# Kernel optimization log

Measured on AMD Instinct MI355X. Metric: run time of the kernel, lower is better.

## Reference

```python
import jax, jax.numpy as jnp
import numpy as np

SIGMA = 1.0  # kernel bandwidth (init kwarg)

VS = 4096   # src vertices
VT = 4096   # tar vertices
FS = 8192   # src triangles
FT = 8192   # tar triangles
FR = 8192   # reference triangles


def setup_inputs() -> dict:
    key = jax.random.key(0)
    k0, k1, k2, k3, k4, k5 = jax.random.split(key, 6)
    src_vertices = jax.random.normal(k0, (VS, 3), dtype=jnp.float32)
    src_indices = jax.random.randint(k1, (FS, 3), 0, VS, dtype=jnp.int64)
    tar_vertices = jax.random.normal(k2, (VT, 3), dtype=jnp.float32)
    tar_indices = jax.random.randint(k3, (FT, 3), 0, VT, dtype=jnp.int64)
    ref_normals = 0.1 * jax.random.normal(k4, (FR, 3), dtype=jnp.float32)
    ref_centers = jax.random.normal(k5, (FR, 3), dtype=jnp.float32)
    return {
        "src_vertices": src_vertices,
        "src_indices": src_indices,
        "tar_vertices": tar_vertices,
        "tar_indices": tar_indices,
        "ref_normals": ref_normals,
        "ref_centers": ref_centers,
    }


def _tri_normals_centers(vertices, indices):
    tris = vertices[indices]               # [F, 3, 3]
    a, b, c = tris[:, 0, :], tris[:, 1, :], tris[:, 2, :]
    normals = 0.5 * jnp.cross(a - b, c - b)  # [F, 3]
    centers = tris.sum(axis=1) / 3.0         # [F, 3]
    return normals, centers


def _sqdist(src, tar):
    # d[i, j] = ||tar_i - src_j||^2  -> shape [Nt, Ns]
    s2 = jnp.sum(src * src, axis=-1)  # [Ns]
    t2 = jnp.sum(tar * tar, axis=-1)  # [Nt]
    return t2[:, None] + s2[None, :] - 2.0 * (tar @ src.T)


def _cauchy(d):
    return 1.0 / (1.0 + d / SIGMA) ** 2


def _energy(sn, sc, tn, tc):
    e1 = jnp.sum((sn @ sn.T) * _cauchy(_sqdist(sc, sc)))
    e2 = jnp.sum((tn @ sn.T) * _cauchy(_sqdist(sc, tc)))
    e3 = jnp.sum((tn @ tn.T) * _cauchy(_sqdist(tc, tc)))
    return e1 - 2.0 * e2 + e3


def reference(src_vertices, src_indices, tar_vertices, tar_indices, ref_normals, ref_centers):
    src_n, src_c = _tri_normals_centers(src_vertices, src_indices)
    tar_n, tar_c = _tri_normals_centers(tar_vertices, tar_indices)
    energy = _energy(src_n, src_c, ref_normals, ref_centers)
    energy = energy + _energy(tar_n, tar_c, ref_normals, ref_centers)
    energy = energy + 0.8 * _energy(src_n, src_c, tar_n, tar_c)
    return energy
```

## Files before the change

### kernel.cpp

```cpp
#include <hip/hip_runtime.h>

#define NSEG 8192
#define NPTS (3 * NSEG)
#define NSUP 96
#define NXB  192
#define NYG  10

typedef short bf16x8 __attribute__((ext_vector_type(8)));
typedef float f32x16 __attribute__((ext_vector_type(16)));
typedef unsigned short u16;

__device__ __forceinline__ u16 f2bf(float x) {
    unsigned u = __builtin_bit_cast(unsigned, x);
    return (u16)((u + 0x7FFFu + ((u >> 16) & 1u)) >> 16);
}
__device__ __forceinline__ float bf2f(u16 h) {
    unsigned u = ((unsigned)h) << 16;
    return __builtin_bit_cast(float, u);
}

__device__ __forceinline__ void compute_point(
    int seg, int f,
    const float* __restrict__ sv, const int* __restrict__ si,
    const float* __restrict__ tv, const int* __restrict__ ti,
    const float* __restrict__ rn, const float* __restrict__ rc,
    float& cx, float& cy, float& cz, float& nx, float& ny, float& nz)
{
    if (seg == 2) {
        nx = rn[3*f];   ny = rn[3*f+1]; nz = rn[3*f+2];
        cx = rc[3*f];   cy = rc[3*f+1]; cz = rc[3*f+2];
    } else {
        const float* v  = (seg == 0) ? sv : tv;
        const int*   nd = (seg == 0) ? si : ti;
        int i0 = nd[3*f], i1 = nd[3*f+1], i2 = nd[3*f+2];
        float ax = v[3*i0], ay = v[3*i0+1], az = v[3*i0+2];
        float bx = v[3*i1], by = v[3*i1+1], bz = v[3*i1+2];
        float gx = v[3*i2], gy = v[3*i2+1], gz = v[3*i2+2];
        float ux = ax-bx, uy = ay-by, uz = az-bz;
        float wx = gx-bx, wy = gy-by, wz = gz-bz;
        nx = 0.5f*(uy*wz - uz*wy);
        ny = 0.5f*(uz*wx - ux*wz);
        nz = 0.5f*(ux*wy - uy*wx);
        cx = (ax+bx+gx)*(1.0f/3.0f);
        cy = (ay+by+gy)*(1.0f/3.0f);
        cz = (az+bz+gz)*(1.0f/3.0f);
    }
}

__global__ void setup_feats(const float* __restrict__ sv, const int* __restrict__ si,
                            const float* __restrict__ tv, const int* __restrict__ ti,
                            const float* __restrict__ rn, const float* __restrict__ rc,
                            u16* __restrict__ ws, float* __restrict__ out) {
    int p = blockIdx.x * 256 + threadIdx.x;
    if (p == 0) out[0] = 0.0f;
    if (p >= NPTS) return;
    int seg = p >> 13, f = p & (NSEG - 1);
    float cx, cy, cz, nx, ny, nz;
    compute_point(seg, f, sv, si, tv, ti, rn, rc, cx, cy, cz, nx, ny, nz);

    const u16 ONE = 0x3F80;
    float s = cx*cx + cy*cy + cz*cz;
    u16 chx = f2bf(cx), chy = f2bf(cy), chz = f2bf(cz);
    u16 clx = f2bf(cx - bf2f(chx)), cly = f2bf(cy - bf2f(chy)), clz = f2bf(cz - bf2f(chz));
    u16 sh  = f2bf(s);
    u16 sl  = f2bf(s - bf2f(sh));
    u16 m2hx = f2bf(-2.0f*bf2f(chx)), m2hy = f2bf(-2.0f*bf2f(chy)), m2hz = f2bf(-2.0f*bf2f(chz));
    u16 m2lx = f2bf(-2.0f*bf2f(clx)), m2ly = f2bf(-2.0f*bf2f(cly)), m2lz = f2bf(-2.0f*bf2f(clz));
    u16 nhx = f2bf(nx), nhy = f2bf(ny), nhz = f2bf(nz);
    u16 nlx = f2bf(nx - bf2f(nhx)), nly = f2bf(ny - bf2f(nhy)), nlz = f2bf(nz - bf2f(nhz));

    u16 at[16] = {chx,chy,chz, clx,cly,clz, chx,chy,chz, sh, sl, ONE, ONE, ONE, 0, 0};
    u16 bt[16] = {m2hx,m2hy,m2hz, m2hx,m2hy,m2hz, m2lx,m2ly,m2lz, ONE, ONE, sh, sl, ONE, 0, 0};
    u16 an[16] = {nhx,nhy,nhz, nlx,nly,nlz, nhx,nhy,nhz, 0,0,0,0,0,0,0};
    u16 bn[16] = {nhx,nhy,nhz, nhx,nhy,nhz, nlx,nly,nlz, 0,0,0,0,0,0,0};

    bf16x8* A8 = (bf16x8*)ws;
    bf16x8* B8 = A8 + (size_t)NPTS*4;
    bf16x8 v0, v1, v2, v3;
    #pragma unroll
    for (int k = 0; k < 8; ++k) { v0[k] = (short)at[k]; v1[k] = (short)at[k+8];
                                  v2[k] = (short)an[k]; v3[k] = (short)an[k+8]; }
    A8[(size_t)p*4+0] = v0; A8[(size_t)p*4+1] = v1; A8[(size_t)p*4+2] = v2; A8[(size_t)p*4+3] = v3;
    #pragma unroll
    for (int k = 0; k < 8; ++k) { v0[k] = (short)bt[k]; v1[k] = (short)bt[k+8];
                                  v2[k] = (short)bn[k]; v3[k] = (short)bn[k+8]; }
    B8[(size_t)p*4+0] = v0; B8[(size_t)p*4+1] = v1; B8[(size_t)p*4+2] = v2; B8[(size_t)p*4+3] = v3;
}

__launch_bounds__(256, 2)
__global__ void energy_mfma(const u16* __restrict__ ws, float* __restrict__ out) {
    const int tid  = threadIdx.x;
    const int lane = tid & 63, wid = tid >> 6;
    const int half = lane >> 5, r32 = lane & 31;

    const int bx = blockIdx.x;
    const int X  = bx >> 1;
    const int g  = blockIdx.y;
    const int y0  = (g < 9) ? 5*g : 45;
    const int ycnt = (g < 9) ? 5 : 4;
    const int gi = X >> 5;

    const bf16x8* A8 = (const bf16x8*)ws;
    const bf16x8* B8 = A8 + (size_t)NPTS*4;

    const int pi = X*256 + (bx & 1)*128 + wid*32 + r32;
    const bf16x8 at = A8[pi*4 + half];
    const bf16x8 an = A8[pi*4 + 2 + half];

    f32x16 Z;
    #pragma unroll
    for (int k = 0; k < 16; ++k) Z[k] = 0.0f;

    const int lofs = r32*4 + half;

    auto yinfo = [&](int y, int& vo, float& w) {
        int J = X + y; if (J >= NSUP) J -= NSUP;
        int jg = J >> 5;
        float base_w;
        if (gi == jg)                 base_w = (gi == 2) ? 2.0f : 1.8f;
        else if (gi == 2 || jg == 2)  base_w = -1.0f;
        else                          base_w = -0.8f;
        const float mult = (y == 0 || y == 48) ? 1.0f : 2.0f;
        w = base_w * mult;
        vo = J*1024 + lofs;
    };

    float acc = 0.0f;
    int vo; float w;
    yinfo(y0, vo, w);

    bf16x8 bt0 = B8[vo],       bn0 = B8[vo + 2];
    bf16x8 bt1 = B8[vo + 128], bn1 = B8[vo + 130];

    #pragma unroll 1
    for (int yy = 0; yy < ycnt; ++yy) {
        int von; float wn;
        yinfo((yy + 1 < ycnt) ? (y0 + yy + 1) : (y0 + yy), von, wn);

        float ts0 = 0.0f, ts1 = 0.0f;
        #pragma unroll 2
        for (int jt = 0; jt < 8; ++jt) {
            const int pofs = (jt < 6) ? (vo + (jt + 2)*128) : (von + (jt - 6)*128);
            bf16x8 pt = B8[pofs];
            bf16x8 pn = B8[pofs + 2];

            f32x16 ct = __builtin_amdgcn_mfma_f32_32x32x16_bf16(at, bt0, Z, 0, 0, 0);
            f32x16 cn = __builtin_amdgcn_mfma_f32_32x32x16_bf16(an, bn0, Z, 0, 0, 0);

            #pragma unroll
            for (int gq = 0; gq < 4; ++gq) {
                float t0 = ct[4*gq+0], t1 = ct[4*gq+1], t2 = ct[4*gq+2], t3 = ct[4*gq+3];
                float q0 = t0*t0, q1 = t1*t1, q2 = t2*t2, q3 = t3*t3;
                float s01 = q0*q1, s23 = q2*q3;
                float r   = __builtin_amdgcn_rcpf(s01*s23);
                float u   = __builtin_fmaf(cn[4*gq+1], q0, cn[4*gq+0]*q1);
                float v   = __builtin_fmaf(cn[4*gq+3], q2, cn[4*gq+2]*q3);
                float num = __builtin_fmaf(v, s01, u*s23);
                if (gq & 1) ts1 = __builtin_fmaf(num, r, ts1);
                else        ts0 = __builtin_fmaf(num, r, ts0);
            }

            bt0 = bt1; bn0 = bn1;
            bt1 = pt;  bn1 = pn;
        }
        acc = __builtin_fmaf(w, ts0 + ts1, acc);
        vo = von; w = wn;
    }

    for (int off = 32; off; off >>= 1) acc += __shfl_down(acc, off, 64);
    __shared__ float partial[4];
    if ((tid & 63) == 0) partial[wid] = acc;
    __syncthreads();
    if (tid == 0)
        atomicAdd(out, (partial[0] + partial[1]) + (partial[2] + partial[3]));
}

extern "C" void kernel_launch(void* const* d_in, const int* in_sizes, int n_in,
                              void* d_out, int out_size, void* d_ws, size_t ws_size,
                              hipStream_t stream) {
    const float* sv = (const float*)d_in[0];
    const int*   si = (const int*)d_in[1];
    const float* tv = (const float*)d_in[2];
    const int*   ti = (const int*)d_in[3];
    const float* rn = (const float*)d_in[4];
    const float* rc = (const float*)d_in[5];
    float* out = (float*)d_out;
    u16*   ws  = (u16*)d_ws;

    setup_feats<<<NPTS/256, 256, 0, stream>>>(sv, si, tv, ti, rn, rc, ws, out);
    dim3 grid(NXB, NYG);
    energy_mfma<<<grid, 256, 0, stream>>>(ws, out);
}
```

Baseline: 114.4 us.

## Process two row tiles per block to reuse B fragments across both

Halves the grid in x and has each wave load two A-row fragments (the two 128-row halves that were previously in separate blocks). Each loaded B fragment now feeds two MFMA pairs and two epilogues, which cuts B global/L2 loads per unit of work in half and amortizes the loop and index overhead. It raises register pressure and reduces the number of blocks, which could lower occupancy or latency hiding.

```diff
diff --git a/kernel.cpp b/kernel.cpp
--- a/kernel.cpp
+++ b/kernel.cpp
@@ -3,7 +3,7 @@
 #define NSEG 8192
 #define NPTS (3 * NSEG)
 #define NSUP 96
-#define NXB  192
+#define NXB  96
 #define NYG  10
 
 typedef short bf16x8 __attribute__((ext_vector_type(8)));
@@ -93,8 +93,7 @@
     const int lane = tid & 63, wid = tid >> 6;
     const int half = lane >> 5, r32 = lane & 31;
 
-    const int bx = blockIdx.x;
-    const int X  = bx >> 1;
+    const int X  = blockIdx.x;
     const int g  = blockIdx.y;
     const int y0  = (g < 9) ? 5*g : 45;
     const int ycnt = (g < 9) ? 5 : 4;
@@ -103,9 +102,11 @@
     const bf16x8* A8 = (const bf16x8*)ws;
     const bf16x8* B8 = A8 + (size_t)NPTS*4;
 
-    const int pi = X*256 + (bx & 1)*128 + wid*32 + r32;
-    const bf16x8 at = A8[pi*4 + half];
-    const bf16x8 an = A8[pi*4 + 2 + half];
+    const int pi = X*256 + wid*32 + r32;
+    const bf16x8 at0 = A8[pi*4 + half];
+    const bf16x8 an0 = A8[pi*4 + 2 + half];
+    const bf16x8 at1 = A8[pi*4 + 512 + half];
+    const bf16x8 an1 = A8[pi*4 + 514 + half];
 
     f32x16 Z;
     #pragma unroll
@@ -125,6 +126,22 @@
         vo = J*1024 + lofs;
     };
 
+#define EPI(CT, CN, TS0, TS1) do {                                            \
+        _Pragma("unroll")                                                     \
+        for (int gq = 0; gq < 4; ++gq) {                                      \
+            float t0 = CT[4*gq+0], t1 = CT[4*gq+1];                           \
+            float t2 = CT[4*gq+2], t3 = CT[4*gq+3];                           \
+            float q0 = t0*t0, q1 = t1*t1, q2 = t2*t2, q3 = t3*t3;             \
+            float s01 = q0*q1, s23 = q2*q3;                                   \
+            float r   = __builtin_amdgcn_rcpf(s01*s23);                       \
+            float u   = __builtin_fmaf(CN[4*gq+1], q0, CN[4*gq+0]*q1);        \
+            float v   = __builtin_fmaf(CN[4*gq+3], q2, CN[4*gq+2]*q3);        \
+            float num = __builtin_fmaf(v, s01, u*s23);                        \
+            if (gq & 1) TS1 = __builtin_fmaf(num, r, TS1);                    \
+            else        TS0 = __builtin_fmaf(num, r, TS0);                    \
+        }                                                                     \
+    } while (0)
+
     float acc = 0.0f;
     int vo; float w;
     yinfo(y0, vo, w);
@@ -137,35 +154,30 @@
         int von; float wn;
         yinfo((yy + 1 < ycnt) ? (y0 + yy + 1) : (y0 + yy), von, wn);
 
-        float ts0 = 0.0f, ts1 = 0.0f;
+        float tsA0 = 0.0f, tsA1 = 0.0f;
+        float tsB0 = 0.0f, tsB1 = 0.0f;
         #pragma unroll 2
         for (int jt = 0; jt < 8; ++jt) {
             const int pofs = (jt < 6) ? (vo + (jt + 2)*128) : (von + (jt - 6)*128);
             bf16x8 pt = B8[pofs];
             bf16x8 pn = B8[pofs + 2];
 
-            f32x16 ct = __builtin_amdgcn_mfma_f32_32x32x16_bf16(at, bt0, Z, 0, 0, 0);
-            f32x16 cn = __builtin_amdgcn_mfma_f32_32x32x16_bf16(an, bn0, Z, 0, 0, 0);
-
-            #pragma unroll
-            for (int gq = 0; gq < 4; ++gq) {
-                float t0 = ct[4*gq+0], t1 = ct[4*gq+1], t2 = ct[4*gq+2], t3 = ct[4*gq+3];
-                float q0 = t0*t0, q1 = t1*t1, q2 = t2*t2, q3 = t3*t3;
-                float s01 = q0*q1, s23 = q2*q3;
-                float r   = __builtin_amdgcn_rcpf(s01*s23);
-                float u   = __builtin_fmaf(cn[4*gq+1], q0, cn[4*gq+0]*q1);
-                float v   = __builtin_fmaf(cn[4*gq+3], q2, cn[4*gq+2]*q3);
-                float num = __builtin_fmaf(v, s01, u*s23);
-                if (gq & 1) ts1 = __builtin_fmaf(num, r, ts1);
-                else        ts0 = __builtin_fmaf(num, r, ts0);
-            }
+            f32x16 ct, cn;
+            ct = __builtin_amdgcn_mfma_f32_32x32x16_bf16(at0, bt0, Z, 0, 0, 0);
+            cn = __builtin_amdgcn_mfma_f32_32x32x16_bf16(an0, bn0, Z, 0, 0, 0);
+            EPI(ct, cn, tsA0, tsA1);
+            ct = __builtin_amdgcn_mfma_f32_32x32x16_bf16(at1, bt0, Z, 0, 0, 0);
+            cn = __builtin_amdgcn_mfma_f32_32x32x16_bf16(an1, bn0, Z, 0, 0, 0);
+            EPI(ct, cn, tsB0, tsB1);
 
             bt0 = bt1; bn0 = bn1;
             bt1 = pt;  bn1 = pn;
         }
-        acc = __builtin_fmaf(w, ts0 + ts1, acc);
+        acc = __builtin_fmaf(w, tsA0 + tsA1, acc);
+        acc = __builtin_fmaf(w, tsB0 + tsB1, acc);
         vo = von; w = wn;
     }
+#undef EPI
 
     for (int off = 32; off; off >>= 1) acc += __shfl_down(acc, off, 64);
     __shared__ float partial[4];
```

New measurement: 114.3 us. Within noise of the previous version (-0.0%).

## Switch energy kernel to 16x16x32 MFMA tiles with four row tiles per wave

Applied to the files above, without the earlier changes.

Replaces the 32x32x16 bf16 MFMA with 16x16x32 MFMA. Each wave now holds four 16-row A tiles in registers and reuses each loaded B fragment across all four, with the unused K half zero-padded. The grid is reshaped from 192x10 to 96x25, so each block covers 256 rows and only 1-2 column supertiles. The aim is smaller accumulators, more B reuse and more parallel blocks, at the cost of wasting half of each MFMA's K dimension and issuing more MFMAs per output.

```diff
diff --git a/kernel.cpp b/kernel.cpp
--- a/kernel.cpp
+++ b/kernel.cpp
@@ -3,11 +3,11 @@
 #define NSEG 8192
 #define NPTS (3 * NSEG)
 #define NSUP 96
-#define NXB  192
-#define NYG  10
+#define NXB  96
+#define NYG  25
 
 typedef short bf16x8 __attribute__((ext_vector_type(8)));
-typedef float f32x16 __attribute__((ext_vector_type(16)));
+typedef float f32x4  __attribute__((ext_vector_type(4)));
 typedef unsigned short u16;
 
 __device__ __forceinline__ u16 f2bf(float x) {
@@ -91,27 +91,34 @@
 __global__ void energy_mfma(const u16* __restrict__ ws, float* __restrict__ out) {
     const int tid  = threadIdx.x;
     const int lane = tid & 63, wid = tid >> 6;
-    const int half = lane >> 5, r32 = lane & 31;
+    const int l15 = lane & 15;
+    const int kg  = lane >> 4;
+    const int kgb = kg & 1;
 
-    const int bx = blockIdx.x;
-    const int X  = bx >> 1;
+    const int X  = blockIdx.x;
     const int g  = blockIdx.y;
-    const int y0  = (g < 9) ? 5*g : 45;
-    const int ycnt = (g < 9) ? 5 : 4;
+    const int y0  = (g < 24) ? 2*g : 48;
+    const int ycnt = (g < 24) ? 2 : 1;
     const int gi = X >> 5;
 
     const bf16x8* A8 = (const bf16x8*)ws;
     const bf16x8* B8 = A8 + (size_t)NPTS*4;
 
-    const int pi = X*256 + (bx & 1)*128 + wid*32 + r32;
-    const bf16x8 at = A8[pi*4 + half];
-    const bf16x8 an = A8[pi*4 + 2 + half];
+    bf16x8 zero8 = (bf16x8){0,0,0,0,0,0,0,0};
+    const int pbase = (X*256 + wid*64 + l15) * 4;
+    bf16x8 at0, an0, at1, an1, at2, an2, at3, an3;
+    if (kg < 2) {
+        at0 = A8[pbase + kg];        an0 = A8[pbase + 2 + kg];
+        at1 = A8[pbase + 64 + kg];   an1 = A8[pbase + 66 + kg];
+        at2 = A8[pbase + 128 + kg];  an2 = A8[pbase + 130 + kg];
+        at3 = A8[pbase + 192 + kg];  an3 = A8[pbase + 194 + kg];
+    } else {
+        at0 = an0 = at1 = an1 = at2 = an2 = at3 = an3 = zero8;
+    }
 
-    f32x16 Z;
-    #pragma unroll
-    for (int k = 0; k < 16; ++k) Z[k] = 0.0f;
+    f32x4 Z = {0.0f, 0.0f, 0.0f, 0.0f};
 
-    const int lofs = r32*4 + half;
+    const int lofsB = l15*4 + kgb;
 
     auto yinfo = [&](int y, int& vo, float& w) {
         int J = X + y; if (J >= NSUP) J -= NSUP;
@@ -122,50 +129,41 @@
         else                          base_w = -0.8f;
         const float mult = (y == 0 || y == 48) ? 1.0f : 2.0f;
         w = base_w * mult;
-        vo = J*1024 + lofs;
+        vo = J*1024 + lofsB;
     };
 
+#define EPIQ(AT, AN, TS) do {                                                 \
+        f32x4 ct = __builtin_amdgcn_mfma_f32_16x16x32_bf16(AT, bt, Z, 0,0,0); \
+        f32x4 cn = __builtin_amdgcn_mfma_f32_16x16x32_bf16(AN, bn, Z, 0,0,0); \
+        float q0 = ct[0]*ct[0], q1 = ct[1]*ct[1];                             \
+        float q2 = ct[2]*ct[2], q3 = ct[3]*ct[3];                             \
+        float s01 = q0*q1, s23 = q2*q3;                                       \
+        float r   = __builtin_amdgcn_rcpf(s01*s23);                           \
+        float u   = __builtin_fmaf(cn[1], q0, cn[0]*q1);                      \
+        float v   = __builtin_fmaf(cn[3], q2, cn[2]*q3);                      \
+        float num = __builtin_fmaf(v, s01, u*s23);                            \
+        TS = __builtin_fmaf(num, r, TS);                                      \
+    } while (0)
+
     float acc = 0.0f;
-    int vo; float w;
-    yinfo(y0, vo, w);
-
-    bf16x8 bt0 = B8[vo],       bn0 = B8[vo + 2];
-    bf16x8 bt1 = B8[vo + 128], bn1 = B8[vo + 130];
-
     #pragma unroll 1
     for (int yy = 0; yy < ycnt; ++yy) {
-        int von; float wn;
-        yinfo((yy + 1 < ycnt) ? (y0 + yy + 1) : (y0 + yy), von, wn);
+        int vo; float w;
+        yinfo(y0 + yy, vo, w);
 
         float ts0 = 0.0f, ts1 = 0.0f;
         #pragma unroll 2
-        for (int jt = 0; jt < 8; ++jt) {
-            const int pofs = (jt < 6) ? (vo + (jt + 2)*128) : (von + (jt - 6)*128);
-            bf16x8 pt = B8[pofs];
-            bf16x8 pn = B8[pofs + 2];
-
-            f32x16 ct = __builtin_amdgcn_mfma_f32_32x32x16_bf16(at, bt0, Z, 0, 0, 0);
-            f32x16 cn = __builtin_amdgcn_mfma_f32_32x32x16_bf16(an, bn0, Z, 0, 0, 0);
-
-            #pragma unroll
-            for (int gq = 0; gq < 4; ++gq) {
-                float t0 = ct[4*gq+0], t1 = ct[4*gq+1], t2 = ct[4*gq+2], t3 = ct[4*gq+3];
-                float q0 = t0*t0, q1 = t1*t1, q2 = t2*t2, q3 = t3*t3;
-                float s01 = q0*q1, s23 = q2*q3;
-                float r   = __builtin_amdgcn_rcpf(s01*s23);
-                float u   = __builtin_fmaf(cn[4*gq+1], q0, cn[4*gq+0]*q1);
-                float v   = __builtin_fmaf(cn[4*gq+3], q2, cn[4*gq+2]*q3);
-                float num = __builtin_fmaf(v, s01, u*s23);
-                if (gq & 1) ts1 = __builtin_fmaf(num, r, ts1);
-                else        ts0 = __builtin_fmaf(num, r, ts0);
-            }
-
-            bt0 = bt1; bn0 = bn1;
-            bt1 = pt;  bn1 = pn;
+        for (int j16 = 0; j16 < 16; ++j16) {
+            bf16x8 bt = B8[vo + j16*64];
+            bf16x8 bn = B8[vo + j16*64 + 2];
+            EPIQ(at0, an0, ts0);
+            EPIQ(at1, an1, ts1);
+            EPIQ(at2, an2, ts0);
+            EPIQ(at3, an3, ts1);
         }
         acc = __builtin_fmaf(w, ts0 + ts1, acc);
-        vo = von; w = wn;
     }
+#undef EPIQ
 
     for (int off = 32; off; off >>= 1) acc += __shfl_down(acc, off, 64);
     __shared__ float partial[4];
```

Result: slower. 119.9 us (+4.8%).
